# Kernel optimization log

Hardware: AMD Instinct MI355X
Metric: run time of the kernel (lower is better)

The kernel has to match this reference:

```python
import jax, jax.numpy as jnp
import numpy as np

B = 128      # batch_size
TF = 80      # video_frame (encoder steps)
DEC = 30     # decoder_length
E = 512      # EmbeddingDim / LSTM hidden size
FEAT = 4096  # video feature dim
V = 6000     # total_words (vocab)


def setup_inputs() -> dict:
    key = jax.random.key(0)
    ks = jax.random.split(key, 13)
    s = 0.05  # weight init scale
    d = {
        "feat": jax.random.normal(ks[0], (B, TF, FEAT), jnp.float32),
        "caption": jax.random.normal(ks[1], (B, DEC, E), jnp.float32),
        "caption_one_hot": jax.random.uniform(ks[2], (B, DEC, V), jnp.float32),
        # LSTMCell 1: input 4096 -> hidden 512 (PyTorch gate order i,f,g,o)
        "w_ih1": jax.random.normal(ks[3], (4 * E, FEAT), jnp.float32) * s,
        "w_hh1": jax.random.normal(ks[4], (4 * E, E), jnp.float32) * s,
        "b_ih1": jax.random.normal(ks[5], (4 * E,), jnp.float32) * s,
        "b_hh1": jax.random.normal(ks[6], (4 * E,), jnp.float32) * s,
        # LSTMCell 2: input 2*512 -> hidden 512
        "w_ih2": jax.random.normal(ks[7], (4 * E, 2 * E), jnp.float32) * s,
        "w_hh2": jax.random.normal(ks[8], (4 * E, E), jnp.float32) * s,
        "b_ih2": jax.random.normal(ks[9], (4 * E,), jnp.float32) * s,
        "b_hh2": jax.random.normal(ks[10], (4 * E,), jnp.float32) * s,
        # output projection to vocab
        "w_out": jax.random.normal(ks[11], (V, E), jnp.float32) * s,
        "b_out": jax.random.normal(ks[12], (V,), jnp.float32) * s,
        "keep_rate": 10,  # coin >= keep_rate never true -> teacher forcing
    }
    return d


def _lstm_cell(x, h, c, w_ih, w_hh, b_ih, b_hh):
    # gates: [B, 4E]; PyTorch LSTMCell gate order (i, f, g, o)
    gates = x @ w_ih.T + h @ w_hh.T + b_ih + b_hh
    i, f, g, o = jnp.split(gates, 4, axis=1)
    c_new = jax.nn.sigmoid(f) * c + jax.nn.sigmoid(i) * jnp.tanh(g)
    h_new = jax.nn.sigmoid(o) * jnp.tanh(c_new)
    return h_new, c_new


def reference(feat, caption, caption_one_hot,
              w_ih1, w_hh1, b_ih1, b_hh1,
              w_ih2, w_hh2, b_ih2, b_hh2,
              w_out, b_out, keep_rate):
    dt = feat.dtype
    pad1 = jnp.zeros((B, FEAT), dt)  # padding_lstm1
    pad2 = jnp.zeros((B, E), dt)     # padding_lstm2

    def enc_step(carry, x):
        h1, c1, h2, c2 = carry
        h1, c1 = _lstm_cell(x, h1, c1, w_ih1, w_hh1, b_ih1, b_hh1)
        h2, c2 = _lstm_cell(jnp.concatenate([pad2, h1], axis=1),
                            h2, c2, w_ih2, w_hh2, b_ih2, b_hh2)
        return (h1, c1, h2, c2), None

    init = tuple(jnp.zeros((B, E), dt) for _ in range(4))
    carry, _ = jax.lax.scan(enc_step, init, jnp.swapaxes(feat, 0, 1))  # [TF,B,FEAT]

    # labels at step+1: argmax over vocab dim (torch.max(caption_one_hot,1)[1])
    labels = jnp.argmax(caption_one_hot, axis=2)  # [B, DEC]

    def dec_step(carry, inp):
        h1, c1, h2, c2 = carry
        x_word, lab = inp  # [B,E], [B]
        h1, c1 = _lstm_cell(pad1, h1, c1, w_ih1, w_hh1, b_ih1, b_hh1)
        h2, c2 = _lstm_cell(jnp.concatenate([x_word, h1], axis=1),
                            h2, c2, w_ih2, w_hh2, b_ih2, b_hh2)
        logits = h2 @ w_out.T + b_out  # [B, V]
        logp = jax.nn.log_softmax(logits, axis=1)
        step_loss = -jnp.take_along_axis(logp, lab[:, None], axis=1)[:, 0]
        return (h1, c1, h2, c2), jnp.sum(step_loss) / B

    xs = (jnp.swapaxes(caption[:, :DEC - 1, :], 0, 1),  # [DEC-1, B, E]
          jnp.swapaxes(labels[:, 1:DEC], 0, 1))         # [DEC-1, B]
    carry, losses = jax.lax.scan(dec_step, carry, xs)
    return jnp.sum(losses).reshape((1,))
```

## Files before the change

### kernel.cpp

```cpp
#include <hip/hip_runtime.h>
#include <cstdint>
#include <cstddef>

#define BB    128
#define TFRM  80
#define DECL  30
#define EE    512
#define FEATD 4096
#define VV    6000
#define VPAD  6016

using frag_ab = __attribute__((ext_vector_type(8))) short;
using frag_cd = __attribute__((ext_vector_type(4))) float;

static __device__ __forceinline__ float sigf(float x)  { return 1.0f / (1.0f + __expf(-x)); }
static __device__ __forceinline__ float tanhf_(float x){ float e = __expf(2.0f * x); return 1.0f - 2.0f / (e + 1.0f); }
static __device__ __forceinline__ unsigned short f2bf_rne(float x) {
    unsigned int u = __float_as_uint(x);
    u += 0x7fffu + ((u >> 16) & 1u);
    return (unsigned short)(u >> 16);
}

__global__ void init_zero(unsigned int* h1a, unsigned int* h1b, unsigned int* h2a, unsigned int* h2b,
                          float* c1, float* c2, float* out) {
    int i = blockIdx.x * blockDim.x + threadIdx.x;
    if (i < 32768) { h1a[i] = 0u; h1b[i] = 0u; h2a[i] = 0u; h2b[i] = 0u; }
    c1[i] = 0.f; c2[i] = 0.f;
    if (i == 0) out[0] = 0.f;
}

__global__ void f2bf(const float* __restrict__ src, unsigned short* __restrict__ dst, int n4) {
    int i = blockIdx.x * blockDim.x + threadIdx.x;
    if (i >= n4) return;
    float4 v = ((const float4*)src)[i];
    ushort4 o;
    o.x = f2bf_rne(v.x); o.y = f2bf_rne(v.y); o.z = f2bf_rne(v.z); o.w = f2bf_rne(v.w);
    ((ushort4*)dst)[i] = o;
}

__global__ void build_wcat2(const float* __restrict__ w_ih2, const float* __restrict__ w_hh2,
                            unsigned short* __restrict__ dst, int n4) {
    int i = blockIdx.x * blockDim.x + threadIdx.x;
    if (i >= n4) return;
    int r  = i >> 8;
    int c  = (i & 255) * 4;
    const float* src = (c < 512) ? (w_ih2 + (size_t)r * 1024 + 512 + c)
                                 : (w_hh2 + (size_t)r * 512 + (c - 512));
    float4 v = *(const float4*)src;
    ushort4 o;
    o.x = f2bf_rne(v.x); o.y = f2bf_rne(v.y); o.z = f2bf_rne(v.z); o.w = f2bf_rne(v.w);
    ((ushort4*)dst)[i] = o;
}

__global__ void wout_pad(const float* __restrict__ w_out, unsigned short* __restrict__ dst, int n4) {
    int i = blockIdx.x * blockDim.x + threadIdx.x;
    if (i >= n4) return;
    int r = i >> 7;
    int c = (i & 127) * 4;
    ushort4 o;
    if (r < VV) {
        float4 v = *(const float4*)(w_out + (size_t)r * EE + c);
        o.x = f2bf_rne(v.x); o.y = f2bf_rne(v.y); o.z = f2bf_rne(v.z); o.w = f2bf_rne(v.w);
    } else {
        o.x = 0; o.y = 0; o.z = 0; o.w = 0;
    }
    ((ushort4*)dst)[i] = o;
}

__global__ void xdec_gather(const float* __restrict__ cap, unsigned short* __restrict__ dst, int n4) {
    int i = blockIdx.x * blockDim.x + threadIdx.x;
    if (i >= n4) return;
    int row = i >> 7;
    int c   = (i & 127) * 4;
    int b = row / 29, t = row - b * 29;
    float4 v = *(const float4*)(cap + (size_t)(b * DECL + t) * EE + c);
    ushort4 o;
    o.x = f2bf_rne(v.x); o.y = f2bf_rne(v.y); o.z = f2bf_rne(v.z); o.w = f2bf_rne(v.w);
    ((ushort4*)dst)[i] = o;
}

__global__ void bias_sum(const float* b_ih1, const float* b_hh1, const float* b_ih2, const float* b_hh2,
                         float* bs1, float* bs2) {
    int i = blockIdx.x * blockDim.x + threadIdx.x;
    bs1[i] = b_ih1[i] + b_hh1[i];
    bs2[i] = b_ih2[i] + b_hh2[i];
}

__global__ void argmax_k(const float* __restrict__ oh, int* __restrict__ labels) {
    int row = blockIdx.x;
    const float* p = oh + (size_t)row * VV;
    int lane = threadIdx.x;
    float best = -1e30f; int bi = 0x7fffffff;
    for (int v = lane; v < VV; v += 64) {
        float x = p[v];
        if (x > best) { best = x; bi = v; }
    }
    for (int off = 32; off; off >>= 1) {
        float ob = __shfl_down(best, off);
        int   oi = __shfl_down(bi,   off);
        if (ob > best || (ob == best && oi < bi)) { best = ob; bi = oi; }
    }
    if (lane == 0) labels[row] = bi;
}

__global__ __launch_bounds__(256) void gemm64(const unsigned short* __restrict__ A, int lda,
                                              const unsigned short* __restrict__ B, int ldb,
                                              float* __restrict__ C, int ldc,
                                              int K, int ntiles,
                                              const float* __restrict__ bias, int biasN) {
    __shared__ unsigned short As[64][40];
    __shared__ unsigned short Bs[64][40];
    int bm = blockIdx.x / ntiles;
    int bn = blockIdx.x % ntiles;
    int tid = threadIdx.x;
    int wave = tid >> 6, lane = tid & 63;

    int srow  = tid >> 2;
    int scol8 = (tid & 3) * 8;
    const unsigned short* Ap = A + (size_t)(bm * 64 + srow) * lda + scol8;
    const unsigned short* Bp = B + (size_t)(bn * 64 + srow) * ldb + scol8;

    frag_cd acc[4] = {};
    int m16 = lane & 15, kg8 = (lane >> 4) * 8;

    for (int k0 = 0; k0 < K; k0 += 32) {
        *(uint4*)&As[srow][scol8] = *(const uint4*)(Ap + k0);
        *(uint4*)&Bs[srow][scol8] = *(const uint4*)(Bp + k0);
        __syncthreads();
        frag_ab bfrag = *(frag_ab*)&Bs[wave * 16 + m16][kg8];
        #pragma unroll
        for (int mt = 0; mt < 4; ++mt) {
            frag_ab afrag = *(frag_ab*)&As[mt * 16 + m16][kg8];
            acc[mt] = __builtin_amdgcn_mfma_f32_16x16x32_bf16(afrag, bfrag, acc[mt], 0, 0, 0);
        }
        __syncthreads();
    }
    int col = bn * 64 + wave * 16 + (lane & 15);
    float bv = 0.f;
    if (bias) bv = (col < biasN) ? bias[col] : 0.f;
    #pragma unroll
    for (int mt = 0; mt < 4; ++mt) {
        int rbase = bm * 64 + mt * 16 + (lane >> 4) * 4;
        #pragma unroll
        for (int i = 0; i < 4; ++i)
            C[(size_t)(rbase + i) * ldc + col] = acc[mt][i] + bv;
    }
}

__global__ __launch_bounds__(256) void lstm_step(const unsigned short* __restrict__ W, int K,
                                                 const unsigned short* __restrict__ Xa,
                                                 const unsigned short* __restrict__ Xb,
                                                 const float* __restrict__ P, int pstride,
                                                 const float* __restrict__ bias,
                                                 float* __restrict__ c,
                                                 unsigned short* __restrict__ hout) {
    __shared__ unsigned short Ws[64][136];
    __shared__ unsigned short Xs[16][136];
    __shared__ float gbuf[4][16][17];

    int et = blockIdx.x >> 3;
    int nt = blockIdx.x & 7;
    int e0 = et * 16, b0 = nt * 16;
    int tid = threadIdx.x;
    int wave = tid >> 6, lane = tid & 63;
    int m16 = lane & 15, kg8 = (lane >> 4) * 8;

    frag_cd acc = {};

    for (int k0 = 0; k0 < K; k0 += 128) {
        #pragma unroll
        for (int p = 0; p < 4; ++p) {
            int lr = p * 16 + (tid >> 4);
            int g = lr >> 4, ei = lr & 15;
            int col8 = (tid & 15) * 8;
            *(uint4*)&Ws[lr][col8] =
                *(const uint4*)(W + (size_t)(g * EE + e0 + ei) * K + k0 + col8);
        }
        {
            int r = tid >> 4;
            int col8 = (tid & 15) * 8;
            const unsigned short* src = (k0 < 512)
                ? (Xa + (size_t)(b0 + r) * EE + k0 + col8)
                : (Xb + (size_t)(b0 + r) * EE + (k0 - 512) + col8);
            *(uint4*)&Xs[r][col8] = *(const uint4*)src;
        }
        __syncthreads();
        #pragma unroll
        for (int kk = 0; kk < 4; ++kk) {
            frag_ab af = *(frag_ab*)&Ws[wave * 16 + m16][kk * 32 + kg8];
            frag_ab bf = *(frag_ab*)&Xs[m16][kk * 32 + kg8];
            acc = __builtin_amdgcn_mfma_f32_16x16x32_bf16(af, bf, acc, 0, 0, 0);
        }
        __syncthreads();
    }

    {
        int er = (lane >> 4) * 4, cb = lane & 15;
        #pragma unroll
        for (int i = 0; i < 4; ++i) gbuf[wave][er + i][cb] = acc[i];
    }
    __syncthreads();

    {
        int e = tid & 15, b = tid >> 4;
        int row = e0 + e;
        int bg  = b0 + b;
        float gi = gbuf[0][e][b] + bias[row];
        float gf = gbuf[1][e][b] + bias[EE + row];
        float gg = gbuf[2][e][b] + bias[2 * EE + row];
        float go = gbuf[3][e][b] + bias[3 * EE + row];
        if (P) {
            const float* pp = P + (size_t)bg * pstride;
            gi += pp[row]; gf += pp[EE + row]; gg += pp[2 * EE + row]; go += pp[3 * EE + row];
        }
        size_t cidx = (size_t)bg * EE + row;
        float cn = sigf(gf) * c[cidx] + sigf(gi) * tanhf_(gg);
        float hn = sigf(go) * tanhf_(cn);
        c[cidx] = cn;
        hout[(size_t)bg * EE + row] = f2bf_rne(hn);
    }
}

__global__ __launch_bounds__(256) void loss_reduce(const float* __restrict__ logits,
                                                   const int* __restrict__ labels,
                                                   int tcol, float* __restrict__ out) {
    __shared__ float red[256];
    int b = blockIdx.x, tid = threadIdx.x;
    const float* lg = logits + (size_t)b * VPAD;
    float mx = -1e30f;
    for (int v = tid; v < VV; v += 256) mx = fmaxf(mx, lg[v]);
    red[tid] = mx; __syncthreads();
    for (int s = 128; s; s >>= 1) {
        if (tid < s) red[tid] = fmaxf(red[tid], red[tid + s]);
        __syncthreads();
    }
    mx = red[0]; __syncthreads();
    float sm = 0.f;
    for (int v = tid; v < VV; v += 256) sm += __expf(lg[v] - mx);
    red[tid] = sm; __syncthreads();
    for (int s = 128; s; s >>= 1) {
        if (tid < s) red[tid] += red[tid + s];
        __syncthreads();
    }
    if (tid == 0) {
        int lab = labels[b * DECL + tcol];
        atomicAdd(out, (mx + __logf(red[0]) - lg[lab]) * (1.0f / BB));
    }
}

extern "C" void kernel_launch(void* const* d_in, const int* in_sizes, int n_in,
                              void* d_out, int out_size, void* d_ws, size_t ws_size,
                              hipStream_t stream) {
    const float* feat    = (const float*)d_in[0];
    const float* caption = (const float*)d_in[1];
    const float* onehot  = (const float*)d_in[2];
    const float* w_ih1   = (const float*)d_in[3];
    const float* w_hh1   = (const float*)d_in[4];
    const float* b_ih1   = (const float*)d_in[5];
    const float* b_hh1   = (const float*)d_in[6];
    const float* w_ih2   = (const float*)d_in[7];
    const float* w_hh2   = (const float*)d_in[8];
    const float* b_ih2   = (const float*)d_in[9];
    const float* b_hh2   = (const float*)d_in[10];
    const float* w_out   = (const float*)d_in[11];
    const float* b_out   = (const float*)d_in[12];
    float* out = (float*)d_out;

    char* ws = (char*)d_ws;
    size_t off = 0;
    auto alloc = [&](size_t bytes) -> char* {
        char* p = ws + off;
        off = (off + bytes + 255) & ~(size_t)255;
        return p;
    };
    unsigned short* feat_bf  = (unsigned short*)alloc((size_t)BB * TFRM * FEATD * 2);
    unsigned short* wih1_bf  = (unsigned short*)alloc((size_t)2048 * FEATD * 2);
    unsigned short* wih2_bf  = (unsigned short*)alloc((size_t)2048 * 1024 * 2);
    unsigned short* whh1_bf  = (unsigned short*)alloc((size_t)2048 * EE * 2);
    unsigned short* wcat2_bf = (unsigned short*)alloc((size_t)2048 * 1024 * 2);
    unsigned short* wout_bf  = (unsigned short*)alloc((size_t)VPAD * EE * 2);
    float* P_enc = (float*)alloc((size_t)BB * TFRM * 2048 * 4);
    float* P_dec = (float*)alloc((size_t)BB * 29 * 2048 * 4);
    unsigned short* xdec_bf = (unsigned short*)alloc((size_t)BB * 29 * EE * 2);
    unsigned short* h1a = (unsigned short*)alloc((size_t)BB * EE * 2);
    unsigned short* h1b = (unsigned short*)alloc((size_t)BB * EE * 2);
    unsigned short* h2a = (unsigned short*)alloc((size_t)BB * EE * 2);
    unsigned short* h2b = (unsigned short*)alloc((size_t)BB * EE * 2);
    float* C1 = (float*)alloc((size_t)BB * EE * 4);
    float* C2 = (float*)alloc((size_t)BB * EE * 4);
    float* logits = (float*)alloc((size_t)BB * VPAD * 4);
    float* bias1 = (float*)alloc(2048 * 4);
    float* bias2 = (float*)alloc(2048 * 4);
    int* labels = (int*)alloc((size_t)BB * DECL * 4);
    if (off > ws_size) return;

    init_zero<<<256, 256, 0, stream>>>((unsigned int*)h1a, (unsigned int*)h1b,
                                       (unsigned int*)h2a, (unsigned int*)h2b, C1, C2, out);
    f2bf<<<40960, 256, 0, stream>>>(feat, feat_bf, BB * TFRM * FEATD / 4);
    f2bf<<<8192, 256, 0, stream>>>(w_ih1, wih1_bf, 2048 * FEATD / 4);
    f2bf<<<2048, 256, 0, stream>>>(w_ih2, wih2_bf, 2048 * 1024 / 4);
    f2bf<<<1024, 256, 0, stream>>>(w_hh1, whh1_bf, 2048 * EE / 4);
    build_wcat2<<<2048, 256, 0, stream>>>(w_ih2, w_hh2, wcat2_bf, 2048 * 1024 / 4);
    wout_pad<<<3008, 256, 0, stream>>>(w_out, wout_bf, VPAD * EE / 4);
    xdec_gather<<<1856, 256, 0, stream>>>(caption, xdec_bf, BB * 29 * EE / 4);
    bias_sum<<<8, 256, 0, stream>>>(b_ih1, b_hh1, b_ih2, b_hh2, bias1, bias2);
    argmax_k<<<BB * DECL, 64, 0, stream>>>(onehot, labels);

    gemm64<<<160 * 32, 256, 0, stream>>>(feat_bf, FEATD, wih1_bf, FEATD, P_enc, 2048,
                                         FEATD, 32, nullptr, 0);
    gemm64<<<58 * 32, 256, 0, stream>>>(xdec_bf, EE, wih2_bf, 1024, P_dec, 2048,
                                        EE, 32, nullptr, 0);

    unsigned short *h1c = h1a, *h1n = h1b, *h2c = h2a, *h2n = h2b;
    for (int t = 0; t < TFRM; ++t) {
        lstm_step<<<256, 256, 0, stream>>>(whh1_bf, EE, h1c, nullptr,
                                           P_enc + (size_t)t * 2048, TFRM * 2048,
                                           bias1, C1, h1n);
        { unsigned short* tmp = h1c; h1c = h1n; h1n = tmp; }
        lstm_step<<<256, 256, 0, stream>>>(wcat2_bf, 1024, h1c, h2c, nullptr, 0,
                                           bias2, C2, h2n);
        { unsigned short* tmp = h2c; h2c = h2n; h2n = tmp; }
    }
    for (int t = 0; t < DECL - 1; ++t) {
        lstm_step<<<256, 256, 0, stream>>>(whh1_bf, EE, h1c, nullptr, nullptr, 0,
                                           bias1, C1, h1n);
        { unsigned short* tmp = h1c; h1c = h1n; h1n = tmp; }
        lstm_step<<<256, 256, 0, stream>>>(wcat2_bf, 1024, h1c, h2c,
                                           P_dec + (size_t)t * 2048, 29 * 2048,
                                           bias2, C2, h2n);
        { unsigned short* tmp = h2c; h2c = h2n; h2n = tmp; }
        gemm64<<<2 * 94, 256, 0, stream>>>(h2c, EE, wout_bf, EE, logits, VPAD,
                                           EE, 94, b_out, VV);
        loss_reduce<<<BB, 256, 0, stream>>>(logits, labels, t + 1, out);
    }
}
```

Measured before the change: 3.059 ms.

## Fuse recurrent LSTM loop into one persistent kernel with grid barriers

Replaces the ~250 per-step kernel launches with a single persistent kernel of 128 blocks. Each block keeps its slice of the recurrent weights resident in LDS and holds the cell state in registers, and steps are separated by atomic-counter grid barriers. The output projection and the loss computation are folded into the same kernel. The input-projection GEMMs move to a 128x128 tile kernel that loads through global_load_lds. This removes launch overhead and repeated weight reloads, at the cost of relying on all 128 blocks being co-resident and of spin-wait barrier latency.

```diff
diff --git a/kernel.cpp b/kernel.cpp
--- a/kernel.cpp
+++ b/kernel.cpp
@@ -9,6 +9,7 @@
 #define FEATD 4096
 #define VV    6000
 #define VPAD  6016
+#define NBLK  128
 
 using frag_ab = __attribute__((ext_vector_type(8))) short;
 using frag_cd = __attribute__((ext_vector_type(4))) float;
@@ -21,12 +22,29 @@
     return (unsigned short)(u >> 16);
 }
 
+static __device__ __forceinline__ void gl_lds16(const unsigned short* g, unsigned short* l) {
+    __builtin_amdgcn_global_load_lds(
+        (const __attribute__((address_space(1))) unsigned int*)g,
+        (__attribute__((address_space(3))) unsigned int*)l, 16, 0, 0);
+}
+
+static __device__ __forceinline__ void gridbar(unsigned int* cnt, unsigned int target) {
+    __syncthreads();
+    if (threadIdx.x == 0) {
+        __threadfence();
+        __hip_atomic_fetch_add(cnt, 1u, __ATOMIC_RELAXED, __HIP_MEMORY_SCOPE_AGENT);
+        while (__hip_atomic_load(cnt, __ATOMIC_RELAXED, __HIP_MEMORY_SCOPE_AGENT) < target)
+            __builtin_amdgcn_s_sleep(1);
+        __threadfence();
+    }
+    __syncthreads();
+}
+
 __global__ void init_zero(unsigned int* h1a, unsigned int* h1b, unsigned int* h2a, unsigned int* h2b,
-                          float* c1, float* c2, float* out) {
-    int i = blockIdx.x * blockDim.x + threadIdx.x;
-    if (i < 32768) { h1a[i] = 0u; h1b[i] = 0u; h2a[i] = 0u; h2b[i] = 0u; }
-    c1[i] = 0.f; c2[i] = 0.f;
-    if (i == 0) out[0] = 0.f;
+                          float* out, unsigned int* barcnt) {
+    int i = blockIdx.x * blockDim.x + threadIdx.x;
+    h1a[i] = 0u; h1b[i] = 0u; h2a[i] = 0u; h2b[i] = 0u;
+    if (i == 0) { out[0] = 0.f; barcnt[0] = 0u; }
 }
 
 __global__ void f2bf(const float* __restrict__ src, unsigned short* __restrict__ dst, int n4) {
@@ -103,148 +121,276 @@
     if (lane == 0) labels[row] = bi;
 }
 
-__global__ __launch_bounds__(256) void gemm64(const unsigned short* __restrict__ A, int lda,
-                                              const unsigned short* __restrict__ B, int ldb,
-                                              float* __restrict__ C, int ldc,
-                                              int K, int ntiles,
-                                              const float* __restrict__ bias, int biasN) {
-    __shared__ unsigned short As[64][40];
-    __shared__ unsigned short Bs[64][40];
-    int bm = blockIdx.x / ntiles;
-    int bn = blockIdx.x % ntiles;
-    int tid = threadIdx.x;
-    int wave = tid >> 6, lane = tid & 63;
-
-    int srow  = tid >> 2;
-    int scol8 = (tid & 3) * 8;
-    const unsigned short* Ap = A + (size_t)(bm * 64 + srow) * lda + scol8;
-    const unsigned short* Bp = B + (size_t)(bn * 64 + srow) * ldb + scol8;
-
-    frag_cd acc[4] = {};
+__global__ __launch_bounds__(256) void gemm128(const unsigned short* __restrict__ A, int lda,
+                                               const unsigned short* __restrict__ B, int ldb,
+                                               float* __restrict__ C, int ldc,
+                                               int K, int ntn) {
+    __shared__ unsigned short As[128][32];
+    __shared__ unsigned short Bs[128][32];
+    int bm = blockIdx.x / ntn, bn = blockIdx.x % ntn;
+    int tid = threadIdx.x, lane = tid & 63, wave = tid >> 6;
+    int wr = (wave >> 1) * 64, wc = (wave & 1) * 64;
     int m16 = lane & 15, kg8 = (lane >> 4) * 8;
-
+    const unsigned short* Ap = A + (size_t)(bm * 128 + (tid >> 2)) * lda + (tid & 3) * 8;
+    const unsigned short* Bp = B + (size_t)(bn * 128 + (tid >> 2)) * ldb + (tid & 3) * 8;
+    unsigned short* Asd = &As[tid >> 2][(tid & 3) * 8];
+    unsigned short* Bsd = &Bs[tid >> 2][(tid & 3) * 8];
+    size_t a64 = (size_t)64 * lda, b64 = (size_t)64 * ldb;
+    frag_cd acc[4][4] = {};
     for (int k0 = 0; k0 < K; k0 += 32) {
-        *(uint4*)&As[srow][scol8] = *(const uint4*)(Ap + k0);
-        *(uint4*)&Bs[srow][scol8] = *(const uint4*)(Bp + k0);
-        __syncthreads();
-        frag_ab bfrag = *(frag_ab*)&Bs[wave * 16 + m16][kg8];
+        gl_lds16(Ap + k0,       Asd);
+        gl_lds16(Ap + a64 + k0, Asd + 64 * 32);
+        gl_lds16(Bp + k0,       Bsd);
+        gl_lds16(Bp + b64 + k0, Bsd + 64 * 32);
+        __syncthreads();
+        frag_ab af[4], bf[4];
         #pragma unroll
-        for (int mt = 0; mt < 4; ++mt) {
-            frag_ab afrag = *(frag_ab*)&As[mt * 16 + m16][kg8];
-            acc[mt] = __builtin_amdgcn_mfma_f32_16x16x32_bf16(afrag, bfrag, acc[mt], 0, 0, 0);
+        for (int i = 0; i < 4; ++i) af[i] = *(const frag_ab*)&As[wr + i * 16 + m16][kg8];
+        #pragma unroll
+        for (int i = 0; i < 4; ++i) bf[i] = *(const frag_ab*)&Bs[wc + i * 16 + m16][kg8];
+        #pragma unroll
+        for (int mt = 0; mt < 4; ++mt)
+            #pragma unroll
+            for (int nt = 0; nt < 4; ++nt)
+                acc[mt][nt] = __builtin_amdgcn_mfma_f32_16x16x32_bf16(af[mt], bf[nt], acc[mt][nt], 0, 0, 0);
+        __syncthreads();
+    }
+    #pragma unroll
+    for (int mt = 0; mt < 4; ++mt) {
+        int r0 = bm * 128 + wr + mt * 16 + (lane >> 4) * 4;
+        #pragma unroll
+        for (int nt = 0; nt < 4; ++nt) {
+            int cc = bn * 128 + wc + nt * 16 + m16;
+            #pragma unroll
+            for (int i = 0; i < 4; ++i)
+                C[(size_t)(r0 + i) * ldc + cc] = acc[mt][nt][i];
         }
-        __syncthreads();
-    }
-    int col = bn * 64 + wave * 16 + (lane & 15);
-    float bv = 0.f;
-    if (bias) bv = (col < biasN) ? bias[col] : 0.f;
-    #pragma unroll
-    for (int mt = 0; mt < 4; ++mt) {
-        int rbase = bm * 64 + mt * 16 + (lane >> 4) * 4;
-        #pragma unroll
-        for (int i = 0; i < 4; ++i)
-            C[(size_t)(rbase + i) * ldc + col] = acc[mt][i] + bv;
-    }
-}
-
-__global__ __launch_bounds__(256) void lstm_step(const unsigned short* __restrict__ W, int K,
-                                                 const unsigned short* __restrict__ Xa,
-                                                 const unsigned short* __restrict__ Xb,
-                                                 const float* __restrict__ P, int pstride,
-                                                 const float* __restrict__ bias,
-                                                 float* __restrict__ c,
-                                                 unsigned short* __restrict__ hout) {
-    __shared__ unsigned short Ws[64][136];
-    __shared__ unsigned short Xs[16][136];
-    __shared__ float gbuf[4][16][17];
-
-    int et = blockIdx.x >> 3;
-    int nt = blockIdx.x & 7;
-    int e0 = et * 16, b0 = nt * 16;
-    int tid = threadIdx.x;
-    int wave = tid >> 6, lane = tid & 63;
+    }
+}
+
+static __device__ __forceinline__ void gemm_gates_512(const unsigned short (*Ws)[520],
+                                                      const unsigned short* __restrict__ hb,
+                                                      float (*gb)[132], int wave, int lane) {
     int m16 = lane & 15, kg8 = (lane >> 4) * 8;
-
-    frag_cd acc = {};
-
-    for (int k0 = 0; k0 < K; k0 += 128) {
-        #pragma unroll
-        for (int p = 0; p < 4; ++p) {
-            int lr = p * 16 + (tid >> 4);
-            int g = lr >> 4, ei = lr & 15;
-            int col8 = (tid & 15) * 8;
-            *(uint4*)&Ws[lr][col8] =
-                *(const uint4*)(W + (size_t)(g * EE + e0 + ei) * K + k0 + col8);
+    frag_cd a0 = {}, a1 = {};
+    const unsigned short* r0 = hb + (size_t)(wave * 32 + m16) * EE + kg8;
+    const unsigned short* r1 = r0 + 16 * EE;
+    #pragma unroll
+    for (int kt = 0; kt < 16; ++kt) {
+        frag_ab af = *(const frag_ab*)&Ws[m16][kt * 32 + kg8];
+        frag_ab b0 = *(const frag_ab*)(r0 + kt * 32);
+        frag_ab b1 = *(const frag_ab*)(r1 + kt * 32);
+        a0 = __builtin_amdgcn_mfma_f32_16x16x32_bf16(af, b0, a0, 0, 0, 0);
+        a1 = __builtin_amdgcn_mfma_f32_16x16x32_bf16(af, b1, a1, 0, 0, 0);
+    }
+    int er = (lane >> 4) * 4;
+    #pragma unroll
+    for (int i = 0; i < 4; ++i) {
+        gb[er + i][wave * 32 + m16]      = a0[i];
+        gb[er + i][wave * 32 + 16 + m16] = a1[i];
+    }
+}
+
+static __device__ __forceinline__ void gemm_gates_1024(const unsigned short (*Ws)[1032],
+                                                       const unsigned short* __restrict__ ha,
+                                                       const unsigned short* __restrict__ hb2,
+                                                       float (*gb)[132], int wave, int lane) {
+    int m16 = lane & 15, kg8 = (lane >> 4) * 8;
+    frag_cd a0 = {}, a1 = {};
+    const unsigned short* r0 = ha + (size_t)(wave * 32 + m16) * EE + kg8;
+    const unsigned short* r1 = r0 + 16 * EE;
+    #pragma unroll
+    for (int kt = 0; kt < 16; ++kt) {
+        frag_ab af = *(const frag_ab*)&Ws[m16][kt * 32 + kg8];
+        frag_ab b0 = *(const frag_ab*)(r0 + kt * 32);
+        frag_ab b1 = *(const frag_ab*)(r1 + kt * 32);
+        a0 = __builtin_amdgcn_mfma_f32_16x16x32_bf16(af, b0, a0, 0, 0, 0);
+        a1 = __builtin_amdgcn_mfma_f32_16x16x32_bf16(af, b1, a1, 0, 0, 0);
+    }
+    const unsigned short* s0 = hb2 + (size_t)(wave * 32 + m16) * EE + kg8;
+    const unsigned short* s1 = s0 + 16 * EE;
+    #pragma unroll
+    for (int kt = 0; kt < 16; ++kt) {
+        frag_ab af = *(const frag_ab*)&Ws[m16][512 + kt * 32 + kg8];
+        frag_ab b0 = *(const frag_ab*)(s0 + kt * 32);
+        frag_ab b1 = *(const frag_ab*)(s1 + kt * 32);
+        a0 = __builtin_amdgcn_mfma_f32_16x16x32_bf16(af, b0, a0, 0, 0, 0);
+        a1 = __builtin_amdgcn_mfma_f32_16x16x32_bf16(af, b1, a1, 0, 0, 0);
+    }
+    int er = (lane >> 4) * 4;
+    #pragma unroll
+    for (int i = 0; i < 4; ++i) {
+        gb[er + i][wave * 32 + m16]      = a0[i];
+        gb[er + i][wave * 32 + 16 + m16] = a1[i];
+    }
+}
+
+static __device__ __forceinline__ void pw_item(float gi, float gf, float gg, float go,
+                                               float& c, unsigned short* h) {
+    float cn = sigf(gf) * c + sigf(gi) * tanhf_(gg);
+    c = cn;
+    *h = f2bf_rne(sigf(go) * tanhf_(cn));
+}
+
+__global__ __launch_bounds__(256, 1) void fused_seq(
+        const unsigned short* __restrict__ W1,
+        const unsigned short* __restrict__ W2,
+        const unsigned short* __restrict__ Wout,
+        const float* __restrict__ bias1, const float* __restrict__ bias2,
+        const float* __restrict__ b_out,
+        const float* __restrict__ P_enc,
+        const float* __restrict__ P_dec,
+        const int* __restrict__ labels,
+        unsigned short* h1a, unsigned short* h1b,
+        unsigned short* h2a, unsigned short* h2b,
+        float* __restrict__ logits,
+        unsigned int* barcnt, float* out) {
+    __shared__ unsigned short W1s[16][520];
+    __shared__ unsigned short W2s[16][1032];
+    __shared__ float gbuf[16][132];
+    __shared__ float red[256];
+
+    int tid = threadIdx.x, lane = tid & 63, wave = tid >> 6;
+    int blk = blockIdx.x;
+    int e0 = blk * 4;
+    int jj = tid & 3, brow = tid >> 2;
+    int m16 = lane & 15, kg8 = (lane >> 4) * 8;
+
+    #pragma unroll
+    for (int i = 0; i < 4; ++i) {
+        int idx = i * 256 + tid;
+        int r = idx >> 6, c8 = (idx & 63) * 8;
+        *(uint4*)&W1s[r][c8] = *(const uint4*)(W1 + (size_t)((r >> 2) * EE + e0 + (r & 3)) * EE + c8);
+    }
+    #pragma unroll
+    for (int i = 0; i < 8; ++i) {
+        int idx = i * 256 + tid;
+        int r = idx >> 7, c8 = (idx & 127) * 8;
+        *(uint4*)&W2s[r][c8] = *(const uint4*)(W2 + (size_t)((r >> 2) * EE + e0 + (r & 3)) * 1024 + c8);
+    }
+    float bs1[4], bs2[4];
+    #pragma unroll
+    for (int g = 0; g < 4; ++g) {
+        bs1[g] = bias1[g * EE + e0 + jj];
+        bs2[g] = bias2[g * EE + e0 + jj];
+    }
+    float c1r0 = 0.f, c1r1 = 0.f, c2r0 = 0.f, c2r1 = 0.f;
+    unsigned short *h1p = h1a, *h1c = h1b, *h2p = h2a, *h2c = h2b;
+    unsigned int bars = 0;
+    __syncthreads();
+
+    for (int t = 0; t < TFRM; ++t) {
+        float pv0[4], pv1[4];
+        {
+            const float* pA = P_enc + ((size_t)(brow * TFRM + t)) * 2048 + e0 + jj;
+            const float* pB = P_enc + ((size_t)((brow + 64) * TFRM + t)) * 2048 + e0 + jj;
+            #pragma unroll
+            for (int g = 0; g < 4; ++g) { pv0[g] = pA[g * EE]; pv1[g] = pB[g * EE]; }
         }
+        gemm_gates_512(W1s, h1p, gbuf, wave, lane);
+        __syncthreads();
+        pw_item(gbuf[jj][brow] + bs1[0] + pv0[0],      gbuf[4 + jj][brow] + bs1[1] + pv0[1],
+                gbuf[8 + jj][brow] + bs1[2] + pv0[2],  gbuf[12 + jj][brow] + bs1[3] + pv0[3],
+                c1r0, &h1c[(size_t)brow * EE + e0 + jj]);
+        pw_item(gbuf[jj][brow + 64] + bs1[0] + pv1[0],     gbuf[4 + jj][brow + 64] + bs1[1] + pv1[1],
+                gbuf[8 + jj][brow + 64] + bs1[2] + pv1[2], gbuf[12 + jj][brow + 64] + bs1[3] + pv1[3],
+                c1r1, &h1c[(size_t)(brow + 64) * EE + e0 + jj]);
+        bars++; gridbar(barcnt, bars * NBLK);
+
+        gemm_gates_1024(W2s, h1c, h2p, gbuf, wave, lane);
+        __syncthreads();
+        pw_item(gbuf[jj][brow] + bs2[0],      gbuf[4 + jj][brow] + bs2[1],
+                gbuf[8 + jj][brow] + bs2[2],  gbuf[12 + jj][brow] + bs2[3],
+                c2r0, &h2c[(size_t)brow * EE + e0 + jj]);
+        pw_item(gbuf[jj][brow + 64] + bs2[0],     gbuf[4 + jj][brow + 64] + bs2[1],
+                gbuf[8 + jj][brow + 64] + bs2[2], gbuf[12 + jj][brow + 64] + bs2[3],
+                c2r1, &h2c[(size_t)(brow + 64) * EE + e0 + jj]);
+        bars++; gridbar(barcnt, bars * NBLK);
+
+        { unsigned short* tmp = h1p; h1p = h1c; h1c = tmp; }
+        { unsigned short* tmp = h2p; h2p = h2c; h2c = tmp; }
+    }
+
+    for (int t = 0; t < DECL - 1; ++t) {
+        gemm_gates_512(W1s, h1p, gbuf, wave, lane);
+        __syncthreads();
+        pw_item(gbuf[jj][brow] + bs1[0],      gbuf[4 + jj][brow] + bs1[1],
+                gbuf[8 + jj][brow] + bs1[2],  gbuf[12 + jj][brow] + bs1[3],
+                c1r0, &h1c[(size_t)brow * EE + e0 + jj]);
+        pw_item(gbuf[jj][brow + 64] + bs1[0],     gbuf[4 + jj][brow + 64] + bs1[1],
+                gbuf[8 + jj][brow + 64] + bs1[2], gbuf[12 + jj][brow + 64] + bs1[3],
+                c1r1, &h1c[(size_t)(brow + 64) * EE + e0 + jj]);
+        bars++; gridbar(barcnt, bars * NBLK);
+
+        float pv0[4], pv1[4];
         {
-            int r = tid >> 4;
-            int col8 = (tid & 15) * 8;
-            const unsigned short* src = (k0 < 512)
-                ? (Xa + (size_t)(b0 + r) * EE + k0 + col8)
-                : (Xb + (size_t)(b0 + r) * EE + (k0 - 512) + col8);
-            *(uint4*)&Xs[r][col8] = *(const uint4*)src;
+            const float* pA = P_dec + ((size_t)(brow * 29 + t)) * 2048 + e0 + jj;
+            const float* pB = P_dec + ((size_t)((brow + 64) * 29 + t)) * 2048 + e0 + jj;
+            #pragma unroll
+            for (int g = 0; g < 4; ++g) { pv0[g] = pA[g * EE]; pv1[g] = pB[g * EE]; }
         }
-        __syncthreads();
-        #pragma unroll
-        for (int kk = 0; kk < 4; ++kk) {
-            frag_ab af = *(frag_ab*)&Ws[wave * 16 + m16][kk * 32 + kg8];
-            frag_ab bf = *(frag_ab*)&Xs[m16][kk * 32 + kg8];
-            acc = __builtin_amdgcn_mfma_f32_16x16x32_bf16(af, bf, acc, 0, 0, 0);
+        gemm_gates_1024(W2s, h1c, h2p, gbuf, wave, lane);
+        __syncthreads();
+        pw_item(gbuf[jj][brow] + bs2[0] + pv0[0],      gbuf[4 + jj][brow] + bs2[1] + pv0[1],
+                gbuf[8 + jj][brow] + bs2[2] + pv0[2],  gbuf[12 + jj][brow] + bs2[3] + pv0[3],
+                c2r0, &h2c[(size_t)brow * EE + e0 + jj]);
+        pw_item(gbuf[jj][brow + 64] + bs2[0] + pv1[0],     gbuf[4 + jj][brow + 64] + bs2[1] + pv1[1],
+                gbuf[8 + jj][brow + 64] + bs2[2] + pv1[2], gbuf[12 + jj][brow + 64] + bs2[3] + pv1[3],
+                c2r1, &h2c[(size_t)(brow + 64) * EE + e0 + jj]);
+        bars++; gridbar(barcnt, bars * NBLK);
+
+        for (int vt = blk; vt < VPAD / 16; vt += NBLK) {
+            frag_cd a0 = {}, a1 = {};
+            const unsigned short* wp = Wout + (size_t)(vt * 16 + m16) * EE + kg8;
+            const unsigned short* r0 = h2c + (size_t)(wave * 32 + m16) * EE + kg8;
+            const unsigned short* r1 = r0 + 16 * EE;
+            #pragma unroll
+            for (int kt = 0; kt < 16; ++kt) {
+                frag_ab af = *(const frag_ab*)(wp + kt * 32);
+                frag_ab b0 = *(const frag_ab*)(r0 + kt * 32);
+                frag_ab b1 = *(const frag_ab*)(r1 + kt * 32);
+                a0 = __builtin_amdgcn_mfma_f32_16x16x32_bf16(af, b0, a0, 0, 0, 0);
+                a1 = __builtin_amdgcn_mfma_f32_16x16x32_bf16(af, b1, a1, 0, 0, 0);
+            }
+            int v0 = vt * 16 + (lane >> 4) * 4;
+            float bb0 = (v0     < VV) ? b_out[v0]     : 0.f;
+            float bb1 = (v0 + 1 < VV) ? b_out[v0 + 1] : 0.f;
+            float bb2 = (v0 + 2 < VV) ? b_out[v0 + 2] : 0.f;
+            float bb3 = (v0 + 3 < VV) ? b_out[v0 + 3] : 0.f;
+            int br0 = wave * 32 + m16;
+            *(float4*)&logits[(size_t)br0 * VPAD + v0] =
+                make_float4(a0[0] + bb0, a0[1] + bb1, a0[2] + bb2, a0[3] + bb3);
+            *(float4*)&logits[(size_t)(br0 + 16) * VPAD + v0] =
+                make_float4(a1[0] + bb0, a1[1] + bb1, a1[2] + bb2, a1[3] + bb3);
         }
-        __syncthreads();
-    }
-
-    {
-        int er = (lane >> 4) * 4, cb = lane & 15;
-        #pragma unroll
-        for (int i = 0; i < 4; ++i) gbuf[wave][er + i][cb] = acc[i];
-    }
-    __syncthreads();
-
-    {
-        int e = tid & 15, b = tid >> 4;
-        int row = e0 + e;
-        int bg  = b0 + b;
-        float gi = gbuf[0][e][b] + bias[row];
-        float gf = gbuf[1][e][b] + bias[EE + row];
-        float gg = gbuf[2][e][b] + bias[2 * EE + row];
-        float go = gbuf[3][e][b] + bias[3 * EE + row];
-        if (P) {
-            const float* pp = P + (size_t)bg * pstride;
-            gi += pp[row]; gf += pp[EE + row]; gg += pp[2 * EE + row]; go += pp[3 * EE + row];
+        bars++; gridbar(barcnt, bars * NBLK);
+
+        {
+            const float* lg = logits + (size_t)blk * VPAD;
+            float mx = -1e30f;
+            for (int v = tid; v < VV; v += 256) mx = fmaxf(mx, lg[v]);
+            red[tid] = mx; __syncthreads();
+            for (int s = 128; s; s >>= 1) {
+                if (tid < s) red[tid] = fmaxf(red[tid], red[tid + s]);
+                __syncthreads();
+            }
+            mx = red[0]; __syncthreads();
+            float sm = 0.f;
+            for (int v = tid; v < VV; v += 256) sm += __expf(lg[v] - mx);
+            red[tid] = sm; __syncthreads();
+            for (int s = 128; s; s >>= 1) {
+                if (tid < s) red[tid] += red[tid + s];
+                __syncthreads();
+            }
+            if (tid == 0) {
+                int lab = labels[blk * DECL + t + 1];
+                atomicAdd(out, (mx + __logf(red[0]) - lg[lab]) * (1.0f / BB));
+            }
+            __syncthreads();
         }
-        size_t cidx = (size_t)bg * EE + row;
-        float cn = sigf(gf) * c[cidx] + sigf(gi) * tanhf_(gg);
-        float hn = sigf(go) * tanhf_(cn);
-        c[cidx] = cn;
-        hout[(size_t)bg * EE + row] = f2bf_rne(hn);
-    }
-}
-
-__global__ __launch_bounds__(256) void loss_reduce(const float* __restrict__ logits,
-                                                   const int* __restrict__ labels,
-                                                   int tcol, float* __restrict__ out) {
-    __shared__ float red[256];
-    int b = blockIdx.x, tid = threadIdx.x;
-    const float* lg = logits + (size_t)b * VPAD;
-    float mx = -1e30f;
-    for (int v = tid; v < VV; v += 256) mx = fmaxf(mx, lg[v]);
-    red[tid] = mx; __syncthreads();
-    for (int s = 128; s; s >>= 1) {
-        if (tid < s) red[tid] = fmaxf(red[tid], red[tid + s]);
-        __syncthreads();
-    }
-    mx = red[0]; __syncthreads();
-    float sm = 0.f;
-    for (int v = tid; v < VV; v += 256) sm += __expf(lg[v] - mx);
-    red[tid] = sm; __syncthreads();
-    for (int s = 128; s; s >>= 1) {
-        if (tid < s) red[tid] += red[tid + s];
-        __syncthreads();
-    }
-    if (tid == 0) {
-        int lab = labels[b * DECL + tcol];
-        atomicAdd(out, (mx + __logf(red[0]) - lg[lab]) * (1.0f / BB));
+
+        { unsigned short* tmp = h1p; h1p = h1c; h1c = tmp; }
+        { unsigned short* tmp = h2p; h2p = h2c; h2c = tmp; }
     }
 }
 
@@ -286,16 +432,15 @@
     unsigned short* h1b = (unsigned short*)alloc((size_t)BB * EE * 2);
     unsigned short* h2a = (unsigned short*)alloc((size_t)BB * EE * 2);
     unsigned short* h2b = (unsigned short*)alloc((size_t)BB * EE * 2);
-    float* C1 = (float*)alloc((size_t)BB * EE * 4);
-    float* C2 = (float*)alloc((size_t)BB * EE * 4);
     float* logits = (float*)alloc((size_t)BB * VPAD * 4);
     float* bias1 = (float*)alloc(2048 * 4);
     float* bias2 = (float*)alloc(2048 * 4);
     int* labels = (int*)alloc((size_t)BB * DECL * 4);
+    unsigned int* barcnt = (unsigned int*)alloc(256);
     if (off > ws_size) return;
 
-    init_zero<<<256, 256, 0, stream>>>((unsigned int*)h1a, (unsigned int*)h1b,
-                                       (unsigned int*)h2a, (unsigned int*)h2b, C1, C2, out);
+    init_zero<<<128, 256, 0, stream>>>((unsigned int*)h1a, (unsigned int*)h1b,
+                                       (unsigned int*)h2a, (unsigned int*)h2b, out, barcnt);
     f2bf<<<40960, 256, 0, stream>>>(feat, feat_bf, BB * TFRM * FEATD / 4);
     f2bf<<<8192, 256, 0, stream>>>(w_ih1, wih1_bf, 2048 * FEATD / 4);
     f2bf<<<2048, 256, 0, stream>>>(w_ih2, wih2_bf, 2048 * 1024 / 4);
@@ -306,31 +451,10 @@
     bias_sum<<<8, 256, 0, stream>>>(b_ih1, b_hh1, b_ih2, b_hh2, bias1, bias2);
     argmax_k<<<BB * DECL, 64, 0, stream>>>(onehot, labels);
 
-    gemm64<<<160 * 32, 256, 0, stream>>>(feat_bf, FEATD, wih1_bf, FEATD, P_enc, 2048,
-                                         FEATD, 32, nullptr, 0);
-    gemm64<<<58 * 32, 256, 0, stream>>>(xdec_bf, EE, wih2_bf, 1024, P_dec, 2048,
-                                        EE, 32, nullptr, 0);
-
-    unsigned short *h1c = h1a, *h1n = h1b, *h2c = h2a, *h2n = h2b;
-    for (int t = 0; t < TFRM; ++t) {
-        lstm_step<<<256, 256, 0, stream>>>(whh1_bf, EE, h1c, nullptr,
-                                           P_enc + (size_t)t * 2048, TFRM * 2048,
-                                           bias1, C1, h1n);
-        { unsigned short* tmp = h1c; h1c = h1n; h1n = tmp; }
-        lstm_step<<<256, 256, 0, stream>>>(wcat2_bf, 1024, h1c, h2c, nullptr, 0,
-                                           bias2, C2, h2n);
-        { unsigned short* tmp = h2c; h2c = h2n; h2n = tmp; }
-    }
-    for (int t = 0; t < DECL - 1; ++t) {
-        lstm_step<<<256, 256, 0, stream>>>(whh1_bf, EE, h1c, nullptr, nullptr, 0,
-                                           bias1, C1, h1n);
-        { unsigned short* tmp = h1c; h1c = h1n; h1n = tmp; }
-        lstm_step<<<256, 256, 0, stream>>>(wcat2_bf, 1024, h1c, h2c,
-                                           P_dec + (size_t)t * 2048, 29 * 2048,
-                                           bias2, C2, h2n);
-        { unsigned short* tmp = h2c; h2c = h2n; h2n = tmp; }
-        gemm64<<<2 * 94, 256, 0, stream>>>(h2c, EE, wout_bf, EE, logits, VPAD,
-                                           EE, 94, b_out, VV);
-        loss_reduce<<<BB, 256, 0, stream>>>(logits, labels, t + 1, out);
-    }
-}
+    gemm128<<<80 * 16, 256, 0, stream>>>(feat_bf, FEATD, wih1_bf, FEATD, P_enc, 2048, FEATD, 16);
+    gemm128<<<29 * 16, 256, 0, stream>>>(xdec_bf, EE, wih2_bf, 1024, P_dec, 2048, EE, 16);
+
+    fused_seq<<<NBLK, 256, 0, stream>>>(whh1_bf, wcat2_bf, wout_bf, bias1, bias2, b_out,
+                                        P_enc, P_dec, labels,
+                                        h1a, h1b, h2a, h2b, logits, barcnt, out);
+}
```

After: 5.356 ms. 1.75x slower.
